# Performance work log

Measured on AMD Instinct MI355X. Metric: run time of the kernel, lower is better.

## Reference

```python
import jax, jax.numpy as jnp
import numpy as np

N = 50000
E = 800000
D = 128          # in_dim = hid_dim = out_dim
R = 8            # num_rels
B = 8            # num_bases
N_LAYERS = 2


def _rgcn_conv(x, basis, comp, root, bias, src, dst, etype):
    """One PyG-style RGCNConv with basis decomposition, mean aggregation per
    relation, root (self-loop) weight and bias.
    x: [N, Din]; basis: [B, Din, Dout]; comp: [R, B]; root: [Din, Dout]; bias: [Dout].
    """
    n = x.shape[0]
    # Relation weights from basis decomposition: W[r] = sum_b comp[r,b] * basis[b]
    W = jnp.einsum('rb,bio->rio', comp, basis)           # [R, Din, Dout]
    # Transform every node under every relation, then gather per-edge message.
    H = jnp.einsum('ni,rio->nro', x, W)                  # [N, R, Dout]
    msg = H[src, etype]                                  # [E, Dout]
    # Per-(dst, relation) in-degree for mean aggregation (PyG aggr='mean').
    deg = jnp.zeros((n, R), x.dtype).at[dst, etype].add(1.0)
    inv = 1.0 / jnp.maximum(deg[dst, etype], 1.0)        # [E]
    agg = jnp.zeros((n, W.shape[2]), x.dtype).at[dst].add(msg * inv[:, None])
    return agg + x @ root + bias


def setup_inputs() -> dict:
    key = jax.random.key(0)
    ks = jax.random.split(key, 3 + 4 * N_LAYERS)
    x = jax.random.normal(ks[0], (N, D), dtype=jnp.float32)
    edge_index = jax.random.randint(ks[1], (2, E), 0, N, dtype=jnp.int64)
    edge_type = jax.random.randint(ks[2], (E,), 0, R, dtype=jnp.int64)
    inp = {'x': x, 'edge_index': edge_index, 'edge_type': edge_type}
    scale = 1.0 / np.sqrt(D)
    for l in range(N_LAYERS):
        k0, k1, k2 = ks[3 + 4 * l], ks[4 + 4 * l], ks[5 + 4 * l]
        inp[f'basis{l}'] = jax.random.normal(k0, (B, D, D), dtype=jnp.float32) * scale
        inp[f'comp{l}'] = jax.random.normal(k1, (R, B), dtype=jnp.float32) * (1.0 / np.sqrt(B))
        inp[f'root{l}'] = jax.random.normal(k2, (D, D), dtype=jnp.float32) * scale
        inp[f'bias{l}'] = jnp.zeros((D,), dtype=jnp.float32)
    return inp


def reference(x, edge_index, edge_type,
              basis0, comp0, root0, bias0,
              basis1, comp1, root1, bias1):
    src, dst = edge_index[0], edge_index[1]
    etype = edge_type
    h = _rgcn_conv(x, basis0, comp0, root0, bias0, src, dst, etype)
    h = jax.nn.relu(h)                 # activation between layers (dropout=0.0)
    h = _rgcn_conv(h, basis1, comp1, root1, bias1, src, dst, etype)
    return h
```

## Files before the change

### kernel.cpp

```cpp
#include <hip/hip_runtime.h>

#define NN 50000
#define EE 800000
#define DD 128
#define RR 8
#define KSTACK 1152
#define NR2 (NN * RR)
#define RPB 32
#define ROWB 2304
#define DUMP16 4608

typedef __attribute__((ext_vector_type(8))) short bf16x8;
typedef __attribute__((ext_vector_type(4))) float f32x4;

__device__ inline float bf2f(ushort u) {
    union { uint i; float f; } v; v.i = ((uint)u) << 16; return v.f;
}
__device__ inline ushort f2bf(float f) {
    uint b = __float_as_uint(f);
    uint r = (b + 0x7fffu + ((b >> 16) & 1u)) >> 16;
    return (ushort)r;
}

__global__ void k_build_w2(const float* __restrict__ b0, const float* __restrict__ c0,
                           const float* __restrict__ r0, const float* __restrict__ b1,
                           const float* __restrict__ c1, const float* __restrict__ r1,
                           ushort* __restrict__ w0, ushort* __restrict__ w1) {
    int idx = blockIdx.x * 256 + threadIdx.x;
    if (idx >= DD * KSTACK) return;
    const float* basis = blockIdx.y ? b1 : b0;
    const float* comp  = blockIdx.y ? c1 : c0;
    const float* root  = blockIdx.y ? r1 : r0;
    ushort* wT         = blockIdx.y ? w1 : w0;
    int o = idx / KSTACK;
    int k = idx % KSTACK;
    float val;
    if (k < RR * DD) {
        int r = k >> 7, i = k & 127;
        float s = 0.f;
        #pragma unroll
        for (int b = 0; b < 8; ++b) s += comp[r * 8 + b] * basis[(b * 128 + i) * 128 + o];
        val = s;
    } else {
        val = root[(k - RR * DD) * 128 + o];
    }
    wT[(size_t)o * KSTACK + k] = f2bf(val);
}

__global__ void k_cvt_bf16(const float* __restrict__ x, ushort* __restrict__ xb, int n4) {
    int i = blockIdx.x * 256 + threadIdx.x;
    if (i < n4) {
        float4 v = ((const float4*)x)[i];
        uint2 p;
        p.x = (uint)f2bf(v.x) | ((uint)f2bf(v.y) << 16);
        p.y = (uint)f2bf(v.z) | ((uint)f2bf(v.w) << 16);
        ((uint2*)xb)[i] = p;
    }
}

__global__ void k_hist(const int* __restrict__ ei, const int* __restrict__ et,
                       int* __restrict__ deg_dr) {
    int e = blockIdx.x * 256 + threadIdx.x;
    if (e < EE) atomicAdd(&deg_dr[ei[EE + e] * RR + et[e]], 1);
}

__device__ inline int rowdeg(const int* __restrict__ deg_dr, int n) {
    int4 a = ((const int4*)deg_dr)[2 * n];
    int4 b = ((const int4*)deg_dr)[2 * n + 1];
    return a.x + a.y + a.z + a.w + b.x + b.y + b.z + b.w;
}

__global__ void k_scan1(const int* __restrict__ deg_dr, int* __restrict__ bsum, int n) {
    __shared__ int s[256];
    int t = threadIdx.x;
    int i = blockIdx.x * 256 + t;
    s[t] = (i < n) ? rowdeg(deg_dr, i) : 0;
    __syncthreads();
    for (int o = 128; o > 0; o >>= 1) {
        if (t < o) s[t] += s[t + o];
        __syncthreads();
    }
    if (t == 0) bsum[blockIdx.x] = s[0];
}

__global__ void k_scan2(int* __restrict__ bsum, int nb) {
    __shared__ int s[256];
    int t = threadIdx.x;
    int v = (t < nb) ? bsum[t] : 0;
    s[t] = v;
    __syncthreads();
    for (int o = 1; o < 256; o <<= 1) {
        int u = (t >= o) ? s[t - o] : 0;
        __syncthreads();
        s[t] += u;
        __syncthreads();
    }
    if (t < nb) bsum[t] = s[t] - v;
}

__global__ void k_scan3(const int* __restrict__ deg_dr, const int* __restrict__ boff,
                        int* __restrict__ ptr, int n) {
    __shared__ int s[256];
    int t = threadIdx.x;
    int i = blockIdx.x * 256 + t;
    int v = (i < n) ? rowdeg(deg_dr, i) : 0;
    s[t] = v;
    __syncthreads();
    for (int o = 1; o < 256; o <<= 1) {
        int u = (t >= o) ? s[t - o] : 0;
        __syncthreads();
        s[t] += u;
        __syncthreads();
    }
    if (i < n) ptr[i + 1] = boff[blockIdx.x] + s[t];
    if (i == 0) ptr[0] = 0;
}

__global__ void k_scatter(const int* __restrict__ ei, const int* __restrict__ et,
                          const int* __restrict__ row_ptr, const int* __restrict__ deg_dr,
                          int* __restrict__ cursor, int2* __restrict__ ekw) {
    int e = blockIdx.x * 256 + threadIdx.x;
    if (e < EE) {
        int s = ei[e], d = ei[EE + e], t = et[e];
        int4 a = ((const int4*)deg_dr)[2 * d];
        int4 b = ((const int4*)deg_dr)[2 * d + 1];
        int pre = 0;
        pre += (t > 0) ? a.x : 0; pre += (t > 1) ? a.y : 0;
        pre += (t > 2) ? a.z : 0; pre += (t > 3) ? a.w : 0;
        pre += (t > 4) ? b.x : 0; pre += (t > 5) ? b.y : 0;
        pre += (t > 6) ? b.z : 0;
        int deg = (t == 0) ? a.x : (t == 1) ? a.y : (t == 2) ? a.z : (t == 3) ? a.w
                : (t == 4) ? b.x : (t == 5) ? b.y : (t == 6) ? b.z : b.w;
        int p = row_ptr[d] + pre + atomicAdd(&cursor[d * RR + t], 1);
        int lrow = d & (RPB - 1);
        int base16 = lrow * (ROWB >> 4) + t * 16;
        int2 pk;
        pk.x = (base16 << 19) | ((lrow & 7) << 16) | s;
        pk.y = __float_as_int(1.f / (float)deg);
        ekw[p] = pk;
    }
}

__global__ void __launch_bounds__(512, 4) k_fused4(
        const ushort* __restrict__ in, const int* __restrict__ rp,
        const int2* __restrict__ ekw, const ushort* __restrict__ BT,
        const float* __restrict__ bias, ushort* __restrict__ hout,
        float* __restrict__ fout) {
    __shared__ uint4 at4[(RPB * ROWB + 256) / 16];
    char* atb = (char*)at4;
    int tid = threadIdx.x, wid = tid >> 6, lane = tid & 63;
    int blockrow = blockIdx.x * RPB;
    uint lane4 = (uint)lane << 2;

    {
        uint4 z = {0u, 0u, 0u, 0u};
        for (int i = tid; i < (RPB * ROWB + 256) / 16; i += 512) at4[i] = z;
    }
    __syncthreads();

    const ushort* inl = in + (lane << 1);

    #pragma unroll
    for (int rr = 0; rr < 4; ++rr) {
        int lr = (wid << 2) + rr;
        int n = blockrow + lr;
        if (n < NN) {
            uint su = *(const uint*)(inl + (size_t)n * DD);
            uint off = (uint)(lr * ROWB + 2048) + (lane4 ^ ((uint)(lr & 7) << 4));
            *(uint*)(atb + off) = su;
        }
    }

    int n0 = blockrow + (wid << 2);
    int i0 = n0 < NN ? n0 : NN;
    int i1 = n0 + 4 < NN ? n0 + 4 : NN;
    int p    = __builtin_amdgcn_readfirstlane(rp[i0]);
    int pend = __builtin_amdgcn_readfirstlane(rp[i1]);
    int nb = pend - p;

    const int U = 8;
    int2 kA[U], kB[U];
    uint gA[U], gB[U];
    float a0 = 0.f, a1 = 0.f;
    uint prev = 0xFFFFFFFFu;

    auto loadc = [&](int2* kb, uint* gb, int base) {
        #pragma unroll
        for (int j = 0; j < U; ++j) {
            int pe = base + j;
            bool dummy = pe >= pend;
            pe = dummy ? (pend - 1) : pe;
            int2 e = ekw[pe];
            if (dummy) { e.x = (int)((uint)DUMP16 << 19); e.y = 0; }
            kb[j] = e;
        }
        #pragma unroll
        for (int j = 0; j < U; ++j)
            gb[j] = *(const uint*)(inl + ((size_t)(kb[j].x & 0xFFFF)) * DD);
    };
    auto proc = [&](int2* kb, uint* gb) {
        #pragma unroll
        for (int j = 0; j < U; ++j) {
            uint ex = (uint)kb[j].x;
            float w = __int_as_float(kb[j].y);
            uint off = ((ex >> 19) << 4) + (lane4 ^ ((ex >> 12) & 0x70u));
            bool same = (off == prev);
            a0 = same ? a0 : 0.f;
            a1 = same ? a1 : 0.f;
            uint g = gb[j];
            a0 += w * bf2f((ushort)(g & 0xFFFFu));
            a1 += w * bf2f((ushort)(g >> 16));
            uint pk;
            asm("v_cvt_pk_bf16_f32 %0, %1, %2" : "=v"(pk) : "v"(a0), "v"(a1));
            *(uint*)(atb + off) = pk;
            prev = off;
        }
    };

    if (nb > 0) {
        int nch = (nb + U - 1) / U;
        loadc(kA, gA, p);
        int i = 1;
        for (; i + 1 < nch; i += 2) {
            loadc(kB, gB, p + i * U);
            proc(kA, gA);
            loadc(kA, gA, p + (i + 1) * U);
            proc(kB, gB);
        }
        if (i < nch) {
            loadc(kB, gB, p + i * U);
            proc(kA, gA);
            proc(kB, gB);
        } else {
            proc(kA, gA);
        }
    }
    __syncthreads();

    int rlo = lane & 15, q = lane >> 4;
    int colbase = wid << 4;
    uint x7 = (uint)(rlo & 7) << 4;
    const char* arow0 = atb + rlo * ROWB;
    const char* arow1 = atb + (rlo + 16) * ROWB;
    const ushort* bp = BT + (size_t)(colbase + rlo) * KSTACK + (q << 3);
    f32x4 c0 = {0.f, 0.f, 0.f, 0.f}, c1 = {0.f, 0.f, 0.f, 0.f};
    #pragma unroll 4
    for (int kk = 0; kk < KSTACK / 32; ++kk) {
        uint loff = (uint)(kk * 64 + q * 16) ^ x7;
        bf16x8 b  = *(const bf16x8*)(bp + kk * 32);
        bf16x8 a0f = *(const bf16x8*)(arow0 + loff);
        bf16x8 a1f = *(const bf16x8*)(arow1 + loff);
        c0 = __builtin_amdgcn_mfma_f32_16x16x32_bf16(a0f, b, c0, 0, 0, 0);
        c1 = __builtin_amdgcn_mfma_f32_16x16x32_bf16(a1f, b, c1, 0, 0, 0);
    }
    int col = colbase + rlo;
    float bv = bias[col];
    int rowoff = q << 2;
    #pragma unroll
    for (int f = 0; f < 2; ++f) {
        f32x4 cv = f ? c1 : c0;
        #pragma unroll
        for (int rg = 0; rg < 4; ++rg) {
            int row = blockrow + f * 16 + rowoff + rg;
            if (row < NN) {
                float v = cv[rg] + bv;
                if (hout) {
                    v = fmaxf(v, 0.f);
                    hout[(size_t)row * DD + col] = f2bf(v);
                } else {
                    fout[(size_t)row * DD + col] = v;
                }
            }
        }
    }
}

extern "C" void kernel_launch(void* const* d_in, const int* in_sizes, int n_in,
                              void* d_out, int out_size, void* d_ws, size_t ws_size,
                              hipStream_t stream) {
    const float* x      = (const float*)d_in[0];
    const int*   ei     = (const int*)d_in[1];
    const int*   et     = (const int*)d_in[2];
    const float* basis0 = (const float*)d_in[3];
    const float* comp0  = (const float*)d_in[4];
    const float* root0  = (const float*)d_in[5];
    const float* bias0  = (const float*)d_in[6];
    const float* basis1 = (const float*)d_in[7];
    const float* comp1  = (const float*)d_in[8];
    const float* root1  = (const float*)d_in[9];
    const float* bias1  = (const float*)d_in[10];
    float* out = (float*)d_out;

    char* ws = (char*)d_ws;
    size_t off = 0;
    auto alloc = [&](size_t bytes) -> void* {
        void* p = ws + off;
        off += (bytes + 255) & ~(size_t)255;
        return p;
    };
    int*    deg_dr  = (int*)alloc((size_t)NR2 * 4);
    int*    cursor  = (int*)alloc((size_t)NR2 * 4);
    size_t zero_bytes = off;
    int*    row_ptr = (int*)alloc((size_t)(NN + 1) * 4);
    int*    bsum    = (int*)alloc(256 * 4);
    int2*   ekw     = (int2*)alloc((size_t)EE * 8);
    ushort* wT0     = (ushort*)alloc((size_t)DD * KSTACK * 2);
    ushort* wT1     = (ushort*)alloc((size_t)DD * KSTACK * 2);
    ushort* xb      = (ushort*)alloc((size_t)NN * DD * 2);
    ushort* h       = (ushort*)alloc((size_t)NN * DD * 2);
    if (off > ws_size) return;

    hipMemsetAsync(d_ws, 0, zero_bytes, stream);

    dim3 wgrid(576, 2);
    k_build_w2<<<wgrid, 256, 0, stream>>>(basis0, comp0, root0, basis1, comp1, root1, wT0, wT1);
    k_cvt_bf16<<<6250, 256, 0, stream>>>(x, xb, NN * DD / 4);
    k_hist<<<3125, 256, 0, stream>>>(ei, et, deg_dr);
    k_scan1<<<196, 256, 0, stream>>>(deg_dr, bsum, NN);
    k_scan2<<<1, 256, 0, stream>>>(bsum, 196);
    k_scan3<<<196, 256, 0, stream>>>(deg_dr, bsum, row_ptr, NN);
    k_scatter<<<3125, 256, 0, stream>>>(ei, et, row_ptr, deg_dr, cursor, ekw);

    int fblocks = (NN + RPB - 1) / RPB;
    k_fused4<<<fblocks, 512, 0, stream>>>(xb, row_ptr, ekw, wT0, bias0, h, nullptr);
    k_fused4<<<fblocks, 512, 0, stream>>>(h, row_ptr, ekw, wT1, bias1, nullptr, out);
}
```

Measured before the change: 309.3 us.

## Halve rows per block in fused RGCN kernel and tile weight-build transpose

The fused aggregate+GEMM kernel now handles 16 destination rows per block instead of 32. Each wave gathers 2 rows instead of 4 and issues one MFMA chain instead of two. This halves LDS per block and raises the launch-bounds occupancy target, to hide gather latency with more resident blocks, at the cost of reading the B weights from global memory twice as often. Separately, the weight-build kernel now stages values in a shared-memory tile so the transposed bf16 stores are coalesced and packed with v_cvt_pk_bf16_f32.

```diff
diff --git a/kernel.cpp b/kernel.cpp
--- a/kernel.cpp
+++ b/kernel.cpp
@@ -6,9 +6,9 @@
 #define RR 8
 #define KSTACK 1152
 #define NR2 (NN * RR)
-#define RPB 32
+#define RPB 16
 #define ROWB 2304
-#define DUMP16 4608
+#define DUMP16 2304
 
 typedef __attribute__((ext_vector_type(8))) short bf16x8;
 typedef __attribute__((ext_vector_type(4))) float f32x4;
@@ -22,29 +22,46 @@
     return (ushort)r;
 }
 
-__global__ void k_build_w2(const float* __restrict__ b0, const float* __restrict__ c0,
-                           const float* __restrict__ r0, const float* __restrict__ b1,
-                           const float* __restrict__ c1, const float* __restrict__ r1,
-                           ushort* __restrict__ w0, ushort* __restrict__ w1) {
-    int idx = blockIdx.x * 256 + threadIdx.x;
-    if (idx >= DD * KSTACK) return;
+__global__ void __launch_bounds__(256) k_build_w3(
+        const float* __restrict__ b0, const float* __restrict__ c0,
+        const float* __restrict__ r0, const float* __restrict__ b1,
+        const float* __restrict__ c1, const float* __restrict__ r1,
+        ushort* __restrict__ w0, ushort* __restrict__ w1) {
+    __shared__ float tile[32][132];
     const float* basis = blockIdx.y ? b1 : b0;
     const float* comp  = blockIdx.y ? c1 : c0;
     const float* root  = blockIdx.y ? r1 : r0;
     ushort* wT         = blockIdx.y ? w1 : w0;
-    int o = idx / KSTACK;
-    int k = idx % KSTACK;
-    float val;
-    if (k < RR * DD) {
-        int r = k >> 7, i = k & 127;
-        float s = 0.f;
-        #pragma unroll
-        for (int b = 0; b < 8; ++b) s += comp[r * 8 + b] * basis[(b * 128 + i) * 128 + o];
-        val = s;
-    } else {
-        val = root[(k - RR * DD) * 128 + o];
-    }
-    wT[(size_t)o * KSTACK + k] = f2bf(val);
+    int tid = threadIdx.x;
+    int k0 = blockIdx.x * 32;
+    #pragma unroll
+    for (int it = 0; it < 16; ++it) {
+        int idx = it * 256 + tid;
+        int kk = idx >> 7, o = idx & 127;
+        int k = k0 + kk;
+        float val;
+        if (k < RR * DD) {
+            int r = k >> 7, i = k & 127;
+            float s = 0.f;
+            #pragma unroll
+            for (int b = 0; b < 8; ++b) s += comp[r * 8 + b] * basis[(b * 128 + i) * 128 + o];
+            val = s;
+        } else {
+            val = root[(k - RR * DD) * 128 + o];
+        }
+        tile[kk][o] = val;
+    }
+    __syncthreads();
+    int o = tid >> 1, half = tid & 1;
+    ushort* wp = wT + (size_t)o * KSTACK + k0 + half * 16;
+    #pragma unroll
+    for (int j = 0; j < 8; ++j) {
+        float lo = tile[half * 16 + 2 * j][o];
+        float hi = tile[half * 16 + 2 * j + 1][o];
+        uint pk;
+        asm("v_cvt_pk_bf16_f32 %0, %1, %2" : "=v"(pk) : "v"(lo), "v"(hi));
+        *(uint*)(wp + 2 * j) = pk;
+    }
 }
 
 __global__ void k_cvt_bf16(const float* __restrict__ x, ushort* __restrict__ xb, int n4) {
@@ -141,7 +158,7 @@
     }
 }
 
-__global__ void __launch_bounds__(512, 4) k_fused4(
+__global__ void __launch_bounds__(512, 8) k_fused5(
         const ushort* __restrict__ in, const int* __restrict__ rp,
         const int2* __restrict__ ekw, const ushort* __restrict__ BT,
         const float* __restrict__ bias, ushort* __restrict__ hout,
@@ -161,8 +178,8 @@
     const ushort* inl = in + (lane << 1);
 
     #pragma unroll
-    for (int rr = 0; rr < 4; ++rr) {
-        int lr = (wid << 2) + rr;
+    for (int rr = 0; rr < 2; ++rr) {
+        int lr = (wid << 1) + rr;
         int n = blockrow + lr;
         if (n < NN) {
             uint su = *(const uint*)(inl + (size_t)n * DD);
@@ -171,9 +188,9 @@
         }
     }
 
-    int n0 = blockrow + (wid << 2);
+    int n0 = blockrow + (wid << 1);
     int i0 = n0 < NN ? n0 : NN;
-    int i1 = n0 + 4 < NN ? n0 + 4 : NN;
+    int i1 = n0 + 2 < NN ? n0 + 2 : NN;
     int p    = __builtin_amdgcn_readfirstlane(rp[i0]);
     int pend = __builtin_amdgcn_readfirstlane(rp[i1]);
     int nb = pend - p;
@@ -240,36 +257,29 @@
     int rlo = lane & 15, q = lane >> 4;
     int colbase = wid << 4;
     uint x7 = (uint)(rlo & 7) << 4;
-    const char* arow0 = atb + rlo * ROWB;
-    const char* arow1 = atb + (rlo + 16) * ROWB;
+    const char* arow = atb + rlo * ROWB;
     const ushort* bp = BT + (size_t)(colbase + rlo) * KSTACK + (q << 3);
-    f32x4 c0 = {0.f, 0.f, 0.f, 0.f}, c1 = {0.f, 0.f, 0.f, 0.f};
+    f32x4 c0 = {0.f, 0.f, 0.f, 0.f};
     #pragma unroll 4
     for (int kk = 0; kk < KSTACK / 32; ++kk) {
         uint loff = (uint)(kk * 64 + q * 16) ^ x7;
         bf16x8 b  = *(const bf16x8*)(bp + kk * 32);
-        bf16x8 a0f = *(const bf16x8*)(arow0 + loff);
-        bf16x8 a1f = *(const bf16x8*)(arow1 + loff);
-        c0 = __builtin_amdgcn_mfma_f32_16x16x32_bf16(a0f, b, c0, 0, 0, 0);
-        c1 = __builtin_amdgcn_mfma_f32_16x16x32_bf16(a1f, b, c1, 0, 0, 0);
+        bf16x8 af = *(const bf16x8*)(arow + loff);
+        c0 = __builtin_amdgcn_mfma_f32_16x16x32_bf16(af, b, c0, 0, 0, 0);
     }
     int col = colbase + rlo;
     float bv = bias[col];
     int rowoff = q << 2;
     #pragma unroll
-    for (int f = 0; f < 2; ++f) {
-        f32x4 cv = f ? c1 : c0;
-        #pragma unroll
-        for (int rg = 0; rg < 4; ++rg) {
-            int row = blockrow + f * 16 + rowoff + rg;
-            if (row < NN) {
-                float v = cv[rg] + bv;
-                if (hout) {
-                    v = fmaxf(v, 0.f);
-                    hout[(size_t)row * DD + col] = f2bf(v);
-                } else {
-                    fout[(size_t)row * DD + col] = v;
-                }
+    for (int rg = 0; rg < 4; ++rg) {
+        int row = blockrow + rowoff + rg;
+        if (row < NN) {
+            float v = c0[rg] + bv;
+            if (hout) {
+                v = fmaxf(v, 0.f);
+                hout[(size_t)row * DD + col] = f2bf(v);
+            } else {
+                fout[(size_t)row * DD + col] = v;
             }
         }
     }
@@ -312,8 +322,8 @@
 
     hipMemsetAsync(d_ws, 0, zero_bytes, stream);
 
-    dim3 wgrid(576, 2);
-    k_build_w2<<<wgrid, 256, 0, stream>>>(basis0, comp0, root0, basis1, comp1, root1, wT0, wT1);
+    dim3 wgrid(KSTACK / 32, 2);
+    k_build_w3<<<wgrid, 256, 0, stream>>>(basis0, comp0, root0, basis1, comp1, root1, wT0, wT1);
     k_cvt_bf16<<<6250, 256, 0, stream>>>(x, xb, NN * DD / 4);
     k_hist<<<3125, 256, 0, stream>>>(ei, et, deg_dr);
     k_scan1<<<196, 256, 0, stream>>>(deg_dr, bsum, NN);
@@ -321,7 +331,7 @@
     k_scan3<<<196, 256, 0, stream>>>(deg_dr, bsum, row_ptr, NN);
     k_scatter<<<3125, 256, 0, stream>>>(ei, et, row_ptr, deg_dr, cursor, ekw);
 
-    int fblocks = (NN + RPB - 1) / RPB;
-    k_fused4<<<fblocks, 512, 0, stream>>>(xb, row_ptr, ekw, wT0, bias0, h, nullptr);
-    k_fused4<<<fblocks, 512, 0, stream>>>(h, row_ptr, ekw, wT1, bias1, nullptr, out);
-}
+    int fblocks = NN / RPB;
+    k_fused5<<<fblocks, 512, 0, stream>>>(xb, row_ptr, ekw, wT0, bias0, h, nullptr);
+    k_fused5<<<fblocks, 512, 0, stream>>>(h, row_ptr, ekw, wT1, bias1, nullptr, out);
+}
```

Measured after the change: 346.5 us. 12.0% more time.

## Load edge records cooperatively per wave and broadcast via readlane; tile weight build

Applied to the files above, without the earlier changes.

The aggregation loop now loads 64 packed edge records per wave with one coalesced vector load, one edge per lane. Each edge's source index and weight is then broadcast with readlane, replacing per-lane redundant scalar-pattern loads of every edge. Feature gathers are issued in 16-edge groups, double-buffered against processing, and the next batch of edge records is prefetched. The weight-building kernel is also restructured to compute through a shared-memory tile and write packed bf16 pairs along K, giving coalesced stores. Segment detection now compares a segment id instead of the LDS offset, and padding edges go to a dump slot.

```diff
diff --git a/kernel.cpp b/kernel.cpp
--- a/kernel.cpp
+++ b/kernel.cpp
@@ -8,7 +8,7 @@
 #define NR2 (NN * RR)
 #define RPB 32
 #define ROWB 2304
-#define DUMP16 4608
+#define DUMPB 73728u
 
 typedef __attribute__((ext_vector_type(8))) short bf16x8;
 typedef __attribute__((ext_vector_type(4))) float f32x4;
@@ -22,29 +22,46 @@
     return (ushort)r;
 }
 
-__global__ void k_build_w2(const float* __restrict__ b0, const float* __restrict__ c0,
-                           const float* __restrict__ r0, const float* __restrict__ b1,
-                           const float* __restrict__ c1, const float* __restrict__ r1,
-                           ushort* __restrict__ w0, ushort* __restrict__ w1) {
-    int idx = blockIdx.x * 256 + threadIdx.x;
-    if (idx >= DD * KSTACK) return;
+__global__ void __launch_bounds__(256) k_build_w3(
+        const float* __restrict__ b0, const float* __restrict__ c0,
+        const float* __restrict__ r0, const float* __restrict__ b1,
+        const float* __restrict__ c1, const float* __restrict__ r1,
+        ushort* __restrict__ w0, ushort* __restrict__ w1) {
+    __shared__ float tile[32][132];
     const float* basis = blockIdx.y ? b1 : b0;
     const float* comp  = blockIdx.y ? c1 : c0;
     const float* root  = blockIdx.y ? r1 : r0;
     ushort* wT         = blockIdx.y ? w1 : w0;
-    int o = idx / KSTACK;
-    int k = idx % KSTACK;
-    float val;
-    if (k < RR * DD) {
-        int r = k >> 7, i = k & 127;
-        float s = 0.f;
-        #pragma unroll
-        for (int b = 0; b < 8; ++b) s += comp[r * 8 + b] * basis[(b * 128 + i) * 128 + o];
-        val = s;
-    } else {
-        val = root[(k - RR * DD) * 128 + o];
-    }
-    wT[(size_t)o * KSTACK + k] = f2bf(val);
+    int tid = threadIdx.x;
+    int k0 = blockIdx.x * 32;
+    #pragma unroll
+    for (int it = 0; it < 16; ++it) {
+        int idx = it * 256 + tid;
+        int kk = idx >> 7, o = idx & 127;
+        int k = k0 + kk;
+        float val;
+        if (k < RR * DD) {
+            int r = k >> 7, i = k & 127;
+            float s = 0.f;
+            #pragma unroll
+            for (int b = 0; b < 8; ++b) s += comp[r * 8 + b] * basis[(b * 128 + i) * 128 + o];
+            val = s;
+        } else {
+            val = root[(k - RR * DD) * 128 + o];
+        }
+        tile[kk][o] = val;
+    }
+    __syncthreads();
+    int o = tid >> 1, half = tid & 1;
+    ushort* wp = wT + (size_t)o * KSTACK + k0 + half * 16;
+    #pragma unroll
+    for (int j = 0; j < 8; ++j) {
+        float lo = tile[half * 16 + 2 * j][o];
+        float hi = tile[half * 16 + 2 * j + 1][o];
+        uint pk;
+        asm("v_cvt_pk_bf16_f32 %0, %1, %2" : "=v"(pk) : "v"(lo), "v"(hi));
+        *(uint*)(wp + 2 * j) = pk;
+    }
 }
 
 __global__ void k_cvt_bf16(const float* __restrict__ x, ushort* __restrict__ xb, int n4) {
@@ -141,7 +158,7 @@
     }
 }
 
-__global__ void __launch_bounds__(512, 4) k_fused4(
+__global__ void __launch_bounds__(512, 4) k_fused6(
         const ushort* __restrict__ in, const int* __restrict__ rp,
         const int2* __restrict__ ekw, const ushort* __restrict__ BT,
         const float* __restrict__ bias, ushort* __restrict__ hout,
@@ -176,64 +193,68 @@
     int i1 = n0 + 4 < NN ? n0 + 4 : NN;
     int p    = __builtin_amdgcn_readfirstlane(rp[i0]);
     int pend = __builtin_amdgcn_readfirstlane(rp[i1]);
-    int nb = pend - p;
-
-    const int U = 8;
-    int2 kA[U], kB[U];
-    uint gA[U], gB[U];
-    float a0 = 0.f, a1 = 0.f;
-    uint prev = 0xFFFFFFFFu;
-
-    auto loadc = [&](int2* kb, uint* gb, int base) {
-        #pragma unroll
-        for (int j = 0; j < U; ++j) {
-            int pe = base + j;
-            bool dummy = pe >= pend;
-            pe = dummy ? (pend - 1) : pe;
-            int2 e = ekw[pe];
-            if (dummy) { e.x = (int)((uint)DUMP16 << 19); e.y = 0; }
-            kb[j] = e;
-        }
-        #pragma unroll
-        for (int j = 0; j < U; ++j)
-            gb[j] = *(const uint*)(inl + ((size_t)(kb[j].x & 0xFFFF)) * DD);
-    };
-    auto proc = [&](int2* kb, uint* gb) {
-        #pragma unroll
-        for (int j = 0; j < U; ++j) {
-            uint ex = (uint)kb[j].x;
-            float w = __int_as_float(kb[j].y);
-            uint off = ((ex >> 19) << 4) + (lane4 ^ ((ex >> 12) & 0x70u));
-            bool same = (off == prev);
-            a0 = same ? a0 : 0.f;
-            a1 = same ? a1 : 0.f;
-            uint g = gb[j];
-            a0 += w * bf2f((ushort)(g & 0xFFFFu));
-            a1 += w * bf2f((ushort)(g >> 16));
-            uint pk;
-            asm("v_cvt_pk_bf16_f32 %0, %1, %2" : "=v"(pk) : "v"(a0), "v"(a1));
-            *(uint*)(atb + off) = pk;
-            prev = off;
-        }
-    };
+    int nb   = pend - p;
 
     if (nb > 0) {
-        int nch = (nb + U - 1) / U;
-        loadc(kA, gA, p);
-        int i = 1;
-        for (; i + 1 < nch; i += 2) {
-            loadc(kB, gB, p + i * U);
-            proc(kA, gA);
-            loadc(kA, gA, p + (i + 1) * U);
-            proc(kB, gB);
-        }
-        if (i < nch) {
-            loadc(kB, gB, p + i * U);
-            proc(kA, gA);
-            proc(kB, gB);
-        } else {
-            proc(kA, gA);
-        }
+        float a0 = 0.f, a1 = 0.f;
+        uint prevsid = 0xFFFFFFFFu;
+        uint g0[16], g1[16];
+        int kvx, kvy, nkvx = 0, nkvy = 0;
+        {
+            int li = lane < nb ? lane : nb - 1;
+            int2 e = ekw[p + li];
+            kvx = e.x; kvy = e.y;
+        }
+        int nbatch = (nb + 63) >> 6;
+
+#define ISSUE(G, CB) \
+        _Pragma("unroll") \
+        for (int j = 0; j < 16; ++j) { \
+            uint sx = (uint)__builtin_amdgcn_readlane(kvx, (CB) + j); \
+            const ushort* src = in + (size_t)(sx & 0xFFFFu) * DD; \
+            G[j] = *(const uint*)(src + (lane << 1)); \
+        }
+#define PROC(G, CB) \
+        _Pragma("unroll") \
+        for (int j = 0; j < 16; ++j) { \
+            uint sx = (uint)__builtin_amdgcn_readlane(kvx, (CB) + j); \
+            int  sy = __builtin_amdgcn_readlane(kvy, (CB) + j); \
+            bool real = ((CB) + j) < rem; \
+            float w = real ? __int_as_float(sy) : 0.f; \
+            uint sid = real ? (sx >> 16) : 0xFFFFFFFFu; \
+            uint offu = real ? ((sx >> 19) << 4) : DUMPB; \
+            uint offv = offu + (lane4 ^ ((sx >> 12) & 0x70u)); \
+            bool same = (sid == prevsid); \
+            a0 = same ? a0 : 0.f; \
+            a1 = same ? a1 : 0.f; \
+            uint g = G[j]; \
+            a0 += w * bf2f((ushort)(g & 0xFFFFu)); \
+            a1 += w * bf2f((ushort)(g >> 16)); \
+            uint pk; \
+            asm("v_cvt_pk_bf16_f32 %0, %1, %2" : "=v"(pk) : "v"(a0), "v"(a1)); \
+            *(uint*)(atb + offv) = pk; \
+            prevsid = sid; \
+        }
+
+        for (int b = 0; b < nbatch; ++b) {
+            int base = p + (b << 6);
+            int rem = pend - base;
+            if (b + 1 < nbatch) {
+                int nbase = base + 64;
+                int nrem = pend - nbase;
+                int li = lane < nrem ? lane : nrem - 1;
+                int2 e = ekw[nbase + li];
+                nkvx = e.x; nkvy = e.y;
+            }
+            ISSUE(g0, 0)
+            ISSUE(g1, 16) PROC(g0, 0)
+            ISSUE(g0, 32) PROC(g1, 16)
+            ISSUE(g1, 48) PROC(g0, 32)
+            PROC(g1, 48)
+            kvx = nkvx; kvy = nkvy;
+        }
+#undef ISSUE
+#undef PROC
     }
     __syncthreads();
 
@@ -247,7 +268,7 @@
     #pragma unroll 4
     for (int kk = 0; kk < KSTACK / 32; ++kk) {
         uint loff = (uint)(kk * 64 + q * 16) ^ x7;
-        bf16x8 b  = *(const bf16x8*)(bp + kk * 32);
+        bf16x8 b   = *(const bf16x8*)(bp + kk * 32);
         bf16x8 a0f = *(const bf16x8*)(arow0 + loff);
         bf16x8 a1f = *(const bf16x8*)(arow1 + loff);
         c0 = __builtin_amdgcn_mfma_f32_16x16x32_bf16(a0f, b, c0, 0, 0, 0);
@@ -312,8 +333,8 @@
 
     hipMemsetAsync(d_ws, 0, zero_bytes, stream);
 
-    dim3 wgrid(576, 2);
-    k_build_w2<<<wgrid, 256, 0, stream>>>(basis0, comp0, root0, basis1, comp1, root1, wT0, wT1);
+    dim3 wgrid(KSTACK / 32, 2);
+    k_build_w3<<<wgrid, 256, 0, stream>>>(basis0, comp0, root0, basis1, comp1, root1, wT0, wT1);
     k_cvt_bf16<<<6250, 256, 0, stream>>>(x, xb, NN * DD / 4);
     k_hist<<<3125, 256, 0, stream>>>(ei, et, deg_dr);
     k_scan1<<<196, 256, 0, stream>>>(deg_dr, bsum, NN);
@@ -322,6 +343,6 @@
     k_scatter<<<3125, 256, 0, stream>>>(ei, et, row_ptr, deg_dr, cursor, ekw);
 
     int fblocks = (NN + RPB - 1) / RPB;
-    k_fused4<<<fblocks, 512, 0, stream>>>(xb, row_ptr, ekw, wT0, bias0, h, nullptr);
-    k_fused4<<<fblocks, 512, 0, stream>>>(h, row_ptr, ekw, wT1, bias1, nullptr, out);
-}
+    k_fused6<<<fblocks, 512, 0, stream>>>(xb, row_ptr, ekw, wT0, bias0, h, nullptr);
+    k_fused6<<<fblocks, 512, 0, stream>>>(h, row_ptr, ekw, wT1, bias1, nullptr, out);
+}
```

After: 325.9 us. 5.4% more time.
